# Kernel optimization log

Measured on AMD Instinct MI355X. Metric: run time of the kernel, lower is better.

Reference implementation:

```python
import jax, jax.numpy as jnp
import numpy as np

B, K, T, C = 4, 8, 2048, 64

def setup_inputs() -> dict:
    key = jax.random.key(0)
    ks = jax.random.split(key, 7)
    return {
        "x": jax.random.normal(ks[0], (B, K, T, C), dtype=jnp.float32),
        "Wq": jax.random.normal(ks[1], (C, C), dtype=jnp.float32) / np.sqrt(C),
        "bq": jax.random.normal(ks[2], (C,), dtype=jnp.float32) * 0.01,
        "Wk": jax.random.normal(ks[3], (C, C), dtype=jnp.float32) / np.sqrt(C),
        "bk": jax.random.normal(ks[4], (C,), dtype=jnp.float32) * 0.01,
        "Wv": jax.random.normal(ks[5], (C, C), dtype=jnp.float32) / np.sqrt(C),
        "bv": jax.random.normal(ks[6], (C,), dtype=jnp.float32) * 0.01,
    }

def reference(x, Wq, bq, Wk, bk, Wv, bv):
    c_dim = x.shape[-1]
    # torch nn.Linear: y = x @ W.T + b
    q = jnp.einsum('bktc,dc->bktd', x, Wq) + bq
    k = jnp.einsum('bktc,dc->bktd', x, Wk) + bk
    v = jnp.einsum('bktc,dc->bktd', x, Wv) + bv
    scores = jnp.einsum('bkic,bkjc->bkij', q, k) / jnp.sqrt(jnp.float32(c_dim))
    attn = jax.nn.softmax(scores, axis=-1)
    out = jnp.einsum('bkij,bkjc->bkic', attn, v)
    return out
```

## Files before the change

kernel.cpp:

```cpp
#include <hip/hip_runtime.h>


#define T_DIM 2048
#define NHEAD 32
#define HSTRIDE (T_DIM * 64)
#define QSCALE 0.18033688011112042f
#define SOFF  8.0f

#define SWZ(row, grp) ((row) * 64 + ((((grp) ^ ((row) & 7)) & 7) * 8))

typedef _Float16 h8 __attribute__((ext_vector_type(8)));
typedef _Float16 h4 __attribute__((ext_vector_type(4)));
typedef __fp16   g2 __attribute__((ext_vector_type(2)));
typedef float    f4 __attribute__((ext_vector_type(4)));

union H4U { h4 v; g2 p[2]; };
union H8U { h8 v; h4 h[2]; };

#if defined(__has_builtin)
#if __has_builtin(__builtin_amdgcn_exp2f)
#define EXP2(x) __builtin_amdgcn_exp2f(x)
#endif
#endif
#ifndef EXP2
__device__ inline float exp2_raw(float x) {
    float r;
    asm("v_exp_f32 %0, %1" : "=v"(r) : "v"(x));
    return r;
}
#define EXP2(x) exp2_raw(x)
#endif

__device__ inline h4 cvt4(f4 x) {
    H4U u;
    u.p[0] = __builtin_amdgcn_cvt_pkrtz(x[0], x[1]);
    u.p[1] = __builtin_amdgcn_cvt_pkrtz(x[2], x[3]);
    return u.v;
}

__global__ __launch_bounds__(256) void qkv_proj_kernel(
    const float* __restrict__ x,
    const float* __restrict__ Wq, const float* __restrict__ bq,
    const float* __restrict__ Wk, const float* __restrict__ bk,
    const float* __restrict__ Wv, const float* __restrict__ bv,
    _Float16* __restrict__ qh, _Float16* __restrict__ khT,
    _Float16* __restrict__ vtT)
{
    __shared__ _Float16 ws[3][64 * 64];
    __shared__ _Float16 xs[64 * 64];
    __shared__ float bsh[3][64];
    _Float16* ot = xs;

    const int tid  = threadIdx.x;
    const int row0 = blockIdx.x * 64;
    const int head = blockIdx.x >> 5;
    const int t0   = (blockIdx.x & 31) * 64;

    #pragma unroll
    for (int m = 0; m < 3; ++m) {
        const float* Wm = (m == 0) ? Wq : ((m == 1) ? Wk : Wv);
        const float* bm = (m == 0) ? bq : ((m == 1) ? bk : bv);
        #pragma unroll
        for (int pass = 0; pass < 4; ++pass) {
            const int idx = pass * 1024 + tid * 4;
            const int d = idx >> 6, c = idx & 63;
            f4 wv = *(const f4*)(Wm + idx);
            *(h4*)&ws[m][SWZ(d, c >> 3) + (c & 7)] = cvt4(wv);
        }
        if (tid < 64) bsh[m][tid] = bm[tid];
    }
    {
        const float* xb = x + (size_t)row0 * 64;
        #pragma unroll
        for (int pass = 0; pass < 4; ++pass) {
            const int idx = pass * 1024 + tid * 4;
            const int r = idx >> 6, c = idx & 63;
            f4 xv = *(const f4*)(xb + idx);
            *(h4*)&xs[SWZ(r, c >> 3) + (c & 7)] = cvt4(xv);
        }
    }
    __syncthreads();

    const int w    = tid >> 6;
    const int lane = tid & 63;
    const int l15  = lane & 15;
    const int qd   = lane >> 4;

    h8 af[2];
    #pragma unroll
    for (int ch = 0; ch < 2; ++ch)
        af[ch] = *(const h8*)&xs[SWZ(w * 16 + l15, ch * 4 + qd)];

    #pragma unroll
    for (int m = 0; m < 3; ++m) {
        h8 bf[4][2];
        #pragma unroll
        for (int ns = 0; ns < 4; ++ns)
            #pragma unroll
            for (int ch = 0; ch < 2; ++ch)
                bf[ns][ch] = *(const h8*)&ws[m][SWZ(ns * 16 + l15, ch * 4 + qd)];

        f4 acc[4];
        #pragma unroll
        for (int ns = 0; ns < 4; ++ns)
            acc[ns] = (f4){0.f, 0.f, 0.f, 0.f};
        #pragma unroll
        for (int ch = 0; ch < 2; ++ch)
            #pragma unroll
            for (int ns = 0; ns < 4; ++ns)
                acc[ns] = __builtin_amdgcn_mfma_f32_16x16x32_f16(
                    af[ch], bf[ns][ch], acc[ns], 0, 0, 0);

        __syncthreads();
        if (m < 2) {
            #pragma unroll
            for (int ns = 0; ns < 4; ++ns) {
                const int d = ns * 16 + l15;
                const float bias = bsh[m][d];
                #pragma unroll
                for (int r = 0; r < 4; ++r) {
                    const int t = w * 16 + qd * 4 + r;
                    float v = acc[ns][r] + bias;
                    if (m == 0) v *= QSCALE;
                    ot[SWZ(t, d >> 3) + (d & 7)] = (_Float16)v;
                }
            }
            __syncthreads();
            if (m == 0) {
                #pragma unroll
                for (int pass = 0; pass < 2; ++pass) {
                    const int t  = pass * 32 + (tid >> 3);
                    const int c0 = (tid & 7) * 8;
                    *(h8*)&qh[(size_t)(row0 + t) * 64 + c0] =
                        *(const h8*)&ot[SWZ(t, tid & 7)];
                }
            } else {
                #pragma unroll
                for (int pass = 0; pass < 2; ++pass) {
                    const int f    = pass * 2048 + tid * 8;
                    const int Jl   = f >> 10;
                    const int rest = f & 1023;
                    const int ch_  = rest >> 9;
                    const int qd_  = (rest >> 7) & 3;
                    const int l15_ = (rest >> 3) & 15;
                    h8 val = *(const h8*)&ot[SWZ(Jl * 16 + l15_, ch_ * 4 + qd_)];
                    *(h8*)&khT[(size_t)head * HSTRIDE + ((t0 >> 4) + Jl) * 1024 + rest] = val;
                }
            }
        } else {
            #pragma unroll
            for (int ns = 0; ns < 4; ++ns) {
                const int d = ns * 16 + l15;
                const float bias = bsh[2][d];
                const int tl = w * 16 + qd * 4;
                f4 pvf;
                #pragma unroll
                for (int r = 0; r < 4; ++r)
                    pvf[r] = acc[ns][r] + bias;
                *(h4*)&ot[SWZ(d, tl >> 3) + (tl & 7)] = cvt4(pvf);
            }
            __syncthreads();
            #pragma unroll
            for (int pass = 0; pass < 2; ++pass) {
                const int f   = pass * 2048 + tid * 8;
                const int qd3 = f >> 10;
                const int rem = f & 1023;
                const int c   = rem >> 4;
                const int g   = (rem & 15) >> 3;
                const int ta  = (2 * g) * 16 + qd3 * 4;
                const int tb  = ta + 16;
                H8U val;
                val.h[0] = *(const h4*)&ot[SWZ(c, ta >> 3) + (ta & 7)];
                val.h[1] = *(const h4*)&ot[SWZ(c, tb >> 3) + (tb & 7)];
                *(h8*)&vtT[(size_t)head * HSTRIDE + (t0 >> 6) * 4096 + f] = val.v;
            }
        }
    }
}

__global__ __launch_bounds__(256, 2) void attn_kernel(
    const _Float16* __restrict__ qh, const _Float16* __restrict__ khT,
    const _Float16* __restrict__ vtT, float* __restrict__ out)
{
    __shared__ float mrg[2][64][41];
    const int tid  = threadIdx.x;
    const int w    = tid >> 6;
    const int lane = tid & 63;
    const int l15  = lane & 15;
    const int qd   = lane >> 4;
    const int qgrp = w >> 1;
    const int kph  = w & 1;

    const int bid  = blockIdx.x;
    const int xcd  = bid & 7;
    const int slot = bid >> 3;
    const int head = xcd * 4 + (slot >> 5);
    const int q0   = (slot & 31) * 64 + qgrp * 32;

    h8 qf[2][2];
    #pragma unroll
    for (int is = 0; is < 2; ++is) {
        const _Float16* qp = qh + (size_t)(head * T_DIM + q0 + is * 16 + l15) * 64 + qd * 8;
        qf[is][0] = *(const h8*)qp;
        qf[is][1] = *(const h8*)(qp + 32);
    }

    const h4 vones = {(_Float16)1.0f, (_Float16)1.0f, (_Float16)1.0f, (_Float16)1.0f};
    f4 lacc[2] = {(f4){0.f,0.f,0.f,0.f}, (f4){0.f,0.f,0.f,0.f}};
    f4 oacc[2][4];
    #pragma unroll
    for (int is = 0; is < 2; ++is)
        #pragma unroll
        for (int cs = 0; cs < 4; ++cs)
            oacc[is][cs] = (f4){0.f, 0.f, 0.f, 0.f};

    const _Float16* kA = khT + (size_t)head * HSTRIDE + kph * 65536;
    const _Float16* kB = kA + 2048;
    const _Float16* vA = vtT + (size_t)head * HSTRIDE + kph * 65536;
    const int ko = lane * 8;
    const int vo = qd * 1024 + l15 * 16;

    h8 kf[4][2];
    #pragma unroll
    for (int jt = 0; jt < 4; ++jt)
        #pragma unroll
        for (int ch = 0; ch < 2; ++ch)
            kf[jt][ch] = *(const h8*)(((jt < 2) ? kA : kB) + (jt & 1) * 1024 + ch * 512 + ko);

    for (int kt = 0; kt < 16; ++kt) {
        H8U vf8[4][2];
        #pragma unroll
        for (int cs = 0; cs < 4; ++cs) {
            vf8[cs][0].v = *(const h8*)(vA + cs * 256 + vo);
            vf8[cs][1].v = *(const h8*)(vA + cs * 256 + vo + 8);
        }

        f4 st[4][2];
        #pragma unroll
        for (int jt = 0; jt < 4; ++jt)
            #pragma unroll
            for (int is = 0; is < 2; ++is)
                st[jt][is] = (f4){-SOFF, -SOFF, -SOFF, -SOFF};
        #pragma unroll
        for (int ch = 0; ch < 2; ++ch)
            #pragma unroll
            for (int jt = 0; jt < 4; ++jt)
                #pragma unroll
                for (int is = 0; is < 2; ++is)
                    st[jt][is] = __builtin_amdgcn_mfma_f32_16x16x32_f16(
                        kf[jt][ch], qf[is][ch], st[jt][is], 0, 0, 0);

        kA += 4096; kB += 4096;
        if (kt < 15) {
            #pragma unroll
            for (int jt = 0; jt < 4; ++jt)
                #pragma unroll
                for (int ch = 0; ch < 2; ++ch)
                    kf[jt][ch] = *(const h8*)(((jt < 2) ? kA : kB) + (jt & 1) * 1024 + ch * 512 + ko);
        }

        h4 pf[4][2];
        #pragma unroll
        for (int is = 0; is < 2; ++is)
            #pragma unroll
            for (int jt = 0; jt < 4; ++jt) {
                f4 p;
                p[0] = EXP2(st[jt][is][0]);
                p[1] = EXP2(st[jt][is][1]);
                p[2] = EXP2(st[jt][is][2]);
                p[3] = EXP2(st[jt][is][3]);
                pf[jt][is] = cvt4(p);
            }

        #pragma unroll
        for (int jt = 0; jt < 4; ++jt) {
            #pragma unroll
            for (int cs = 0; cs < 4; ++cs)
                #pragma unroll
                for (int is = 0; is < 2; ++is)
                    oacc[is][cs] = __builtin_amdgcn_mfma_f32_16x16x16f16(
                        pf[jt][is], vf8[cs][jt >> 1].h[jt & 1], oacc[is][cs], 0, 0, 0);
            #pragma unroll
            for (int is = 0; is < 2; ++is)
                lacc[is] = __builtin_amdgcn_mfma_f32_16x16x16f16(
                    pf[jt][is], vones, lacc[is], 0, 0, 0);
        }
        vA += 4096;
    }

    if (kph == 1) {
        #pragma unroll
        for (int is = 0; is < 2; ++is) {
            #pragma unroll
            for (int cs = 0; cs < 4; ++cs)
                #pragma unroll
                for (int r = 0; r < 4; ++r)
                    mrg[qgrp][lane][(is * 4 + cs) * 4 + r] = oacc[is][cs][r];
            #pragma unroll
            for (int r = 0; r < 4; ++r)
                mrg[qgrp][lane][32 + is * 4 + r] = lacc[is][r];
        }
    }
    __syncthreads();
    if (kph == 0) {
        #pragma unroll
        for (int is = 0; is < 2; ++is) {
            float linv[4];
            #pragma unroll
            for (int r = 0; r < 4; ++r)
                linv[r] = 1.f / (lacc[is][r] + mrg[qgrp][lane][32 + is * 4 + r]);
            #pragma unroll
            for (int cs = 0; cs < 4; ++cs) {
                const int c = cs * 16 + l15;
                #pragma unroll
                for (int r = 0; r < 4; ++r) {
                    const int t = q0 + is * 16 + qd * 4 + r;
                    float o = oacc[is][cs][r] + mrg[qgrp][lane][(is * 4 + cs) * 4 + r];
                    out[(size_t)(head * T_DIM + t) * 64 + c] = o * linv[r];
                }
            }
        }
    }
}

extern "C" void kernel_launch(void* const* d_in, const int* in_sizes, int n_in,
                              void* d_out, int out_size, void* d_ws, size_t ws_size,
                              hipStream_t stream)
{
    (void)in_sizes; (void)n_in; (void)out_size; (void)ws_size;
    const float* x  = (const float*)d_in[0];
    const float* Wq = (const float*)d_in[1];
    const float* bq = (const float*)d_in[2];
    const float* Wk = (const float*)d_in[3];
    const float* bk = (const float*)d_in[4];
    const float* Wv = (const float*)d_in[5];
    const float* bv = (const float*)d_in[6];
    float* out = (float*)d_out;

    _Float16* qh  = (_Float16*)d_ws;
    _Float16* khT = qh + (size_t)NHEAD * HSTRIDE;
    _Float16* vtT = khT + (size_t)NHEAD * HSTRIDE;

    hipLaunchKernelGGL(qkv_proj_kernel, dim3(1024), dim3(256), 0, stream,
                       x, Wq, bq, Wk, bk, Wv, bv, qh, khT, vtT);
    hipLaunchKernelGGL(attn_kernel, dim3(1024), dim3(256), 0, stream,
                       qh, khT, vtT, out);
}
```

Before: 131.0 us.

## Split attention key range across four waves per query group and load x directly

The attention kernel now launches 512 threads per block, so each query group has four waves, each handling a quarter of the key sequence (8 tiles instead of 16). Partial outputs and row sums are merged through shared memory in three sequential rounds. The aim is shorter per-wave serial loops and more waves in flight to hide latency, at the cost of more merge synchronisation and register pressure under the 512-thread launch bound. Separately, the QKV projection loads x straight from global memory into MFMA fragments instead of staging it through shared memory.

```diff
diff --git a/kernel.cpp b/kernel.cpp
--- a/kernel.cpp
+++ b/kernel.cpp
@@ -38,6 +38,13 @@
     return u.v;
 }
 
+__device__ inline h8 cvt8(f4 a, f4 b) {
+    H8U r;
+    r.h[0] = cvt4(a);
+    r.h[1] = cvt4(b);
+    return r.v;
+}
+
 __global__ __launch_bounds__(256) void qkv_proj_kernel(
     const float* __restrict__ x,
     const float* __restrict__ Wq, const float* __restrict__ bq,
@@ -47,9 +54,8 @@
     _Float16* __restrict__ vtT)
 {
     __shared__ _Float16 ws[3][64 * 64];
-    __shared__ _Float16 xs[64 * 64];
+    __shared__ _Float16 ot[64 * 64];
     __shared__ float bsh[3][64];
-    _Float16* ot = xs;
 
     const int tid  = threadIdx.x;
     const int row0 = blockIdx.x * 64;
@@ -69,17 +75,6 @@
         }
         if (tid < 64) bsh[m][tid] = bm[tid];
     }
-    {
-        const float* xb = x + (size_t)row0 * 64;
-        #pragma unroll
-        for (int pass = 0; pass < 4; ++pass) {
-            const int idx = pass * 1024 + tid * 4;
-            const int r = idx >> 6, c = idx & 63;
-            f4 xv = *(const f4*)(xb + idx);
-            *(h4*)&xs[SWZ(r, c >> 3) + (c & 7)] = cvt4(xv);
-        }
-    }
-    __syncthreads();
 
     const int w    = tid >> 6;
     const int lane = tid & 63;
@@ -87,9 +82,16 @@
     const int qd   = lane >> 4;
 
     h8 af[2];
-    #pragma unroll
-    for (int ch = 0; ch < 2; ++ch)
-        af[ch] = *(const h8*)&xs[SWZ(w * 16 + l15, ch * 4 + qd)];
+    {
+        const float* xp = x + (size_t)(row0 + w * 16 + l15) * 64 + qd * 8;
+        #pragma unroll
+        for (int ch = 0; ch < 2; ++ch) {
+            f4 a0 = *(const f4*)(xp + ch * 32);
+            f4 a1 = *(const f4*)(xp + ch * 32 + 4);
+            af[ch] = cvt8(a0, a1);
+        }
+    }
+    __syncthreads();
 
     #pragma unroll
     for (int m = 0; m < 3; ++m) {
@@ -178,7 +180,7 @@
     }
 }
 
-__global__ __launch_bounds__(256, 2) void attn_kernel(
+__global__ __launch_bounds__(512, 2) void attn_kernel(
     const _Float16* __restrict__ qh, const _Float16* __restrict__ khT,
     const _Float16* __restrict__ vtT, float* __restrict__ out)
 {
@@ -188,8 +190,8 @@
     const int lane = tid & 63;
     const int l15  = lane & 15;
     const int qd   = lane >> 4;
-    const int qgrp = w >> 1;
-    const int kph  = w & 1;
+    const int qgrp = w & 1;
+    const int kph  = w >> 1;
 
     const int bid  = blockIdx.x;
     const int xcd  = bid & 7;
@@ -214,9 +216,9 @@
         for (int cs = 0; cs < 4; ++cs)
             oacc[is][cs] = (f4){0.f, 0.f, 0.f, 0.f};
 
-    const _Float16* kA = khT + (size_t)head * HSTRIDE + kph * 65536;
+    const _Float16* kA = khT + (size_t)head * HSTRIDE + kph * 32768;
     const _Float16* kB = kA + 2048;
-    const _Float16* vA = vtT + (size_t)head * HSTRIDE + kph * 65536;
+    const _Float16* vA = vtT + (size_t)head * HSTRIDE + kph * 32768;
     const int ko = lane * 8;
     const int vo = qd * 1024 + l15 * 16;
 
@@ -227,7 +229,7 @@
         for (int ch = 0; ch < 2; ++ch)
             kf[jt][ch] = *(const h8*)(((jt < 2) ? kA : kB) + (jt & 1) * 1024 + ch * 512 + ko);
 
-    for (int kt = 0; kt < 16; ++kt) {
+    for (int kt = 0; kt < 8; ++kt) {
         H8U vf8[4][2];
         #pragma unroll
         for (int cs = 0; cs < 4; ++cs) {
@@ -251,7 +253,7 @@
                         kf[jt][ch], qf[is][ch], st[jt][is], 0, 0, 0);
 
         kA += 4096; kB += 4096;
-        if (kt < 15) {
+        if (kt < 7) {
             #pragma unroll
             for (int jt = 0; jt < 4; ++jt)
                 #pragma unroll
@@ -288,35 +290,52 @@
         vA += 4096;
     }
 
-    if (kph == 1) {
-        #pragma unroll
-        for (int is = 0; is < 2; ++is) {
-            #pragma unroll
-            for (int cs = 0; cs < 4; ++cs)
+    #pragma unroll
+    for (int src = 3; src >= 1; --src) {
+        if (kph == src) {
+            #pragma unroll
+            for (int is = 0; is < 2; ++is) {
+                #pragma unroll
+                for (int cs = 0; cs < 4; ++cs)
+                    #pragma unroll
+                    for (int r = 0; r < 4; ++r)
+                        mrg[qgrp][lane][(is * 4 + cs) * 4 + r] = oacc[is][cs][r];
                 #pragma unroll
                 for (int r = 0; r < 4; ++r)
-                    mrg[qgrp][lane][(is * 4 + cs) * 4 + r] = oacc[is][cs][r];
-            #pragma unroll
-            for (int r = 0; r < 4; ++r)
-                mrg[qgrp][lane][32 + is * 4 + r] = lacc[is][r];
-        }
-    }
-    __syncthreads();
+                    mrg[qgrp][lane][32 + is * 4 + r] = lacc[is][r];
+            }
+        }
+        __syncthreads();
+        if (kph == 0) {
+            #pragma unroll
+            for (int is = 0; is < 2; ++is) {
+                #pragma unroll
+                for (int cs = 0; cs < 4; ++cs)
+                    #pragma unroll
+                    for (int r = 0; r < 4; ++r)
+                        oacc[is][cs][r] += mrg[qgrp][lane][(is * 4 + cs) * 4 + r];
+                #pragma unroll
+                for (int r = 0; r < 4; ++r)
+                    lacc[is][r] += mrg[qgrp][lane][32 + is * 4 + r];
+            }
+        }
+        if (src > 1) __syncthreads();
+    }
+
     if (kph == 0) {
         #pragma unroll
         for (int is = 0; is < 2; ++is) {
             float linv[4];
             #pragma unroll
             for (int r = 0; r < 4; ++r)
-                linv[r] = 1.f / (lacc[is][r] + mrg[qgrp][lane][32 + is * 4 + r]);
+                linv[r] = 1.f / lacc[is][r];
             #pragma unroll
             for (int cs = 0; cs < 4; ++cs) {
                 const int c = cs * 16 + l15;
                 #pragma unroll
                 for (int r = 0; r < 4; ++r) {
                     const int t = q0 + is * 16 + qd * 4 + r;
-                    float o = oacc[is][cs][r] + mrg[qgrp][lane][(is * 4 + cs) * 4 + r];
-                    out[(size_t)(head * T_DIM + t) * 64 + c] = o * linv[r];
+                    out[(size_t)(head * T_DIM + t) * 64 + c] = oacc[is][cs][r] * linv[r];
                 }
             }
         }
@@ -343,6 +362,6 @@
 
     hipLaunchKernelGGL(qkv_proj_kernel, dim3(1024), dim3(256), 0, stream,
                        x, Wq, bq, Wk, bk, Wv, bv, qh, khT, vtT);
-    hipLaunchKernelGGL(attn_kernel, dim3(1024), dim3(256), 0, stream,
+    hipLaunchKernelGGL(attn_kernel, dim3(1024), dim3(512), 0, stream,
                        qh, khT, vtT, out);
 }
```

New measurement: 132.9 us. About the same (+1.5%).

## Switch attention to 32x32x16 MFMA tiles with shuffled P fragments and new K/V layouts

Applied to the files above, without the earlier changes.

Rewrites the attention inner loop to use 32x32x16 f16 MFMA for both QK^T and PV. The P fragment is rebuilt via lane-xor-32 shuffles instead of going through LDS, and the row sum is computed with scalar adds instead of an extra ones-MFMA. The projection kernel writes K and V in new tile layouts matching the 32x32 operand order and loads x straight from global into registers. Occupancy hint rises to 3 blocks per CU. The larger tiles cut instruction count and drop the ones-MFMA, but the shuffles and selects add VALU work and register pressure.

```diff
diff --git a/kernel.cpp b/kernel.cpp
--- a/kernel.cpp
+++ b/kernel.cpp
@@ -13,9 +13,12 @@
 typedef _Float16 h4 __attribute__((ext_vector_type(4)));
 typedef __fp16   g2 __attribute__((ext_vector_type(2)));
 typedef float    f4 __attribute__((ext_vector_type(4)));
+typedef float    f16v __attribute__((ext_vector_type(16)));
 
 union H4U { h4 v; g2 p[2]; };
 union H8U { h8 v; h4 h[2]; };
+union PKU { g2 g; unsigned u; };
+union FRU { h8 v; unsigned u[4]; };
 
 #if defined(__has_builtin)
 #if __has_builtin(__builtin_amdgcn_exp2f)
@@ -38,6 +41,13 @@
     return u.v;
 }
 
+__device__ inline h8 cvt8(f4 a, f4 b) {
+    H8U r;
+    r.h[0] = cvt4(a);
+    r.h[1] = cvt4(b);
+    return r.v;
+}
+
 __global__ __launch_bounds__(256) void qkv_proj_kernel(
     const float* __restrict__ x,
     const float* __restrict__ Wq, const float* __restrict__ bq,
@@ -47,14 +57,13 @@
     _Float16* __restrict__ vtT)
 {
     __shared__ _Float16 ws[3][64 * 64];
-    __shared__ _Float16 xs[64 * 64];
+    __shared__ _Float16 ot[64 * 64];
     __shared__ float bsh[3][64];
-    _Float16* ot = xs;
 
     const int tid  = threadIdx.x;
     const int row0 = blockIdx.x * 64;
     const int head = blockIdx.x >> 5;
-    const int t0   = (blockIdx.x & 31) * 64;
+    const int kt0  = blockIdx.x & 31;
 
     #pragma unroll
     for (int m = 0; m < 3; ++m) {
@@ -69,17 +78,6 @@
         }
         if (tid < 64) bsh[m][tid] = bm[tid];
     }
-    {
-        const float* xb = x + (size_t)row0 * 64;
-        #pragma unroll
-        for (int pass = 0; pass < 4; ++pass) {
-            const int idx = pass * 1024 + tid * 4;
-            const int r = idx >> 6, c = idx & 63;
-            f4 xv = *(const f4*)(xb + idx);
-            *(h4*)&xs[SWZ(r, c >> 3) + (c & 7)] = cvt4(xv);
-        }
-    }
-    __syncthreads();
 
     const int w    = tid >> 6;
     const int lane = tid & 63;
@@ -87,9 +85,16 @@
     const int qd   = lane >> 4;
 
     h8 af[2];
-    #pragma unroll
-    for (int ch = 0; ch < 2; ++ch)
-        af[ch] = *(const h8*)&xs[SWZ(w * 16 + l15, ch * 4 + qd)];
+    {
+        const float* xp = x + (size_t)(row0 + w * 16 + l15) * 64 + qd * 8;
+        #pragma unroll
+        for (int ch = 0; ch < 2; ++ch) {
+            f4 a0 = *(const f4*)(xp + ch * 32);
+            f4 a1 = *(const f4*)(xp + ch * 32 + 4);
+            af[ch] = cvt8(a0, a1);
+        }
+    }
+    __syncthreads();
 
     #pragma unroll
     for (int m = 0; m < 3; ++m) {
@@ -137,14 +142,14 @@
             } else {
                 #pragma unroll
                 for (int pass = 0; pass < 2; ++pass) {
-                    const int f    = pass * 2048 + tid * 8;
-                    const int Jl   = f >> 10;
-                    const int rest = f & 1023;
-                    const int ch_  = rest >> 9;
-                    const int qd_  = (rest >> 7) & 3;
-                    const int l15_ = (rest >> 3) & 15;
-                    h8 val = *(const h8*)&ot[SWZ(Jl * 16 + l15_, ch_ * 4 + qd_)];
-                    *(h8*)&khT[(size_t)head * HSTRIDE + ((t0 >> 4) + Jl) * 1024 + rest] = val;
+                    const int f  = pass * 2048 + tid * 8;
+                    const int r  = f >> 9;
+                    const int l  = (f >> 3) & 63;
+                    const int jb = r >> 2, kc = r & 3;
+                    const int jl = jb * 32 + (l & 31);
+                    const int cg = kc * 2 + (l >> 5);
+                    h8 val = *(const h8*)&ot[SWZ(jl, cg)];
+                    *(h8*)&khT[(size_t)head * HSTRIDE + kt0 * 4096 + f] = val;
                 }
             }
         } else {
@@ -162,32 +167,29 @@
             __syncthreads();
             #pragma unroll
             for (int pass = 0; pass < 2; ++pass) {
-                const int f   = pass * 2048 + tid * 8;
-                const int qd3 = f >> 10;
-                const int rem = f & 1023;
-                const int c   = rem >> 4;
-                const int g   = (rem & 15) >> 3;
-                const int ta  = (2 * g) * 16 + qd3 * 4;
-                const int tb  = ta + 16;
-                H8U val;
-                val.h[0] = *(const h4*)&ot[SWZ(c, ta >> 3) + (ta & 7)];
-                val.h[1] = *(const h4*)&ot[SWZ(c, tb >> 3) + (tb & 7)];
-                *(h8*)&vtT[(size_t)head * HSTRIDE + (t0 >> 6) * 4096 + f] = val.v;
-            }
-        }
-    }
-}
-
-__global__ __launch_bounds__(256, 2) void attn_kernel(
+                const int f  = pass * 2048 + tid * 8;
+                const int r  = f >> 9;
+                const int l  = (f >> 3) & 63;
+                const int jc = r >> 1, cb = r & 1;
+                const int c  = cb * 32 + (l & 31);
+                const int tg = jc * 2 + (l >> 5);
+                h8 val = *(const h8*)&ot[SWZ(c, tg)];
+                *(h8*)&vtT[(size_t)head * HSTRIDE + kt0 * 4096 + f] = val;
+            }
+        }
+    }
+}
+
+__global__ __launch_bounds__(256, 3) void attn_kernel(
     const _Float16* __restrict__ qh, const _Float16* __restrict__ khT,
     const _Float16* __restrict__ vtT, float* __restrict__ out)
 {
-    __shared__ float mrg[2][64][41];
+    __shared__ float mrg[2][64][33];
     const int tid  = threadIdx.x;
     const int w    = tid >> 6;
     const int lane = tid & 63;
-    const int l15  = lane & 15;
-    const int qd   = lane >> 4;
+    const int i32  = lane & 31;
+    const int hl   = lane >> 5;
     const int qgrp = w >> 1;
     const int kph  = w & 1;
 
@@ -197,128 +199,123 @@
     const int head = xcd * 4 + (slot >> 5);
     const int q0   = (slot & 31) * 64 + qgrp * 32;
 
-    h8 qf[2][2];
+    h8 qf[4];
+    {
+        const _Float16* qp = qh + (size_t)(head * T_DIM + q0 + i32) * 64 + hl * 8;
+        #pragma unroll
+        for (int kc = 0; kc < 4; ++kc)
+            qf[kc] = *(const h8*)(qp + kc * 16);
+    }
+
+    f16v oacc[2];
     #pragma unroll
-    for (int is = 0; is < 2; ++is) {
-        const _Float16* qp = qh + (size_t)(head * T_DIM + q0 + is * 16 + l15) * 64 + qd * 8;
-        qf[is][0] = *(const h8*)qp;
-        qf[is][1] = *(const h8*)(qp + 32);
-    }
-
-    const h4 vones = {(_Float16)1.0f, (_Float16)1.0f, (_Float16)1.0f, (_Float16)1.0f};
-    f4 lacc[2] = {(f4){0.f,0.f,0.f,0.f}, (f4){0.f,0.f,0.f,0.f}};
-    f4 oacc[2][4];
+    for (int cb = 0; cb < 2; ++cb)
+        #pragma unroll
+        for (int e = 0; e < 16; ++e)
+            oacc[cb][e] = 0.f;
+    float lsum = 0.f;
+
+    const _Float16* kA = khT + (size_t)head * HSTRIDE + kph * 16 * 4096;
+    const _Float16* kB = kA + 2048;
+    const _Float16* vA = vtT + (size_t)head * HSTRIDE + kph * 16 * 4096;
+    const _Float16* vB = vA + 2048;
+    const int ko = lane * 8;
+
+    h8 kf[8];
     #pragma unroll
-    for (int is = 0; is < 2; ++is)
-        #pragma unroll
-        for (int cs = 0; cs < 4; ++cs)
-            oacc[is][cs] = (f4){0.f, 0.f, 0.f, 0.f};
-
-    const _Float16* kA = khT + (size_t)head * HSTRIDE + kph * 65536;
-    const _Float16* kB = kA + 2048;
-    const _Float16* vA = vtT + (size_t)head * HSTRIDE + kph * 65536;
-    const int ko = lane * 8;
-    const int vo = qd * 1024 + l15 * 16;
-
-    h8 kf[4][2];
-    #pragma unroll
-    for (int jt = 0; jt < 4; ++jt)
-        #pragma unroll
-        for (int ch = 0; ch < 2; ++ch)
-            kf[jt][ch] = *(const h8*)(((jt < 2) ? kA : kB) + (jt & 1) * 1024 + ch * 512 + ko);
+    for (int r = 0; r < 8; ++r)
+        kf[r] = *(const h8*)(((r < 4) ? kA : kB) + (r & 3) * 512 + ko);
 
     for (int kt = 0; kt < 16; ++kt) {
-        H8U vf8[4][2];
-        #pragma unroll
-        for (int cs = 0; cs < 4; ++cs) {
-            vf8[cs][0].v = *(const h8*)(vA + cs * 256 + vo);
-            vf8[cs][1].v = *(const h8*)(vA + cs * 256 + vo + 8);
-        }
-
-        f4 st[4][2];
-        #pragma unroll
-        for (int jt = 0; jt < 4; ++jt)
-            #pragma unroll
-            for (int is = 0; is < 2; ++is)
-                st[jt][is] = (f4){-SOFF, -SOFF, -SOFF, -SOFF};
-        #pragma unroll
-        for (int ch = 0; ch < 2; ++ch)
-            #pragma unroll
-            for (int jt = 0; jt < 4; ++jt)
-                #pragma unroll
-                for (int is = 0; is < 2; ++is)
-                    st[jt][is] = __builtin_amdgcn_mfma_f32_16x16x32_f16(
-                        kf[jt][ch], qf[is][ch], st[jt][is], 0, 0, 0);
+        h8 vf[8];
+        #pragma unroll
+        for (int r = 0; r < 8; ++r)
+            vf[r] = *(const h8*)(((r < 4) ? vA : vB) + (r & 3) * 512 + ko);
+
+        f16v st[2];
+        #pragma unroll
+        for (int jb = 0; jb < 2; ++jb)
+            #pragma unroll
+            for (int e = 0; e < 16; ++e)
+                st[jb][e] = -SOFF;
+        #pragma unroll
+        for (int kc = 0; kc < 4; ++kc)
+            #pragma unroll
+            for (int jb = 0; jb < 2; ++jb)
+                st[jb] = __builtin_amdgcn_mfma_f32_32x32x16_f16(
+                    kf[jb * 4 + kc], qf[kc], st[jb], 0, 0, 0);
 
         kA += 4096; kB += 4096;
         if (kt < 15) {
             #pragma unroll
-            for (int jt = 0; jt < 4; ++jt)
-                #pragma unroll
-                for (int ch = 0; ch < 2; ++ch)
-                    kf[jt][ch] = *(const h8*)(((jt < 2) ? kA : kB) + (jt & 1) * 1024 + ch * 512 + ko);
-        }
-
-        h4 pf[4][2];
-        #pragma unroll
-        for (int is = 0; is < 2; ++is)
-            #pragma unroll
-            for (int jt = 0; jt < 4; ++jt) {
-                f4 p;
-                p[0] = EXP2(st[jt][is][0]);
-                p[1] = EXP2(st[jt][is][1]);
-                p[2] = EXP2(st[jt][is][2]);
-                p[3] = EXP2(st[jt][is][3]);
-                pf[jt][is] = cvt4(p);
-            }
-
-        #pragma unroll
-        for (int jt = 0; jt < 4; ++jt) {
-            #pragma unroll
-            for (int cs = 0; cs < 4; ++cs)
-                #pragma unroll
-                for (int is = 0; is < 2; ++is)
-                    oacc[is][cs] = __builtin_amdgcn_mfma_f32_16x16x16f16(
-                        pf[jt][is], vf8[cs][jt >> 1].h[jt & 1], oacc[is][cs], 0, 0, 0);
-            #pragma unroll
-            for (int is = 0; is < 2; ++is)
-                lacc[is] = __builtin_amdgcn_mfma_f32_16x16x16f16(
-                    pf[jt][is], vones, lacc[is], 0, 0, 0);
-        }
-        vA += 4096;
-    }
+            for (int r = 0; r < 8; ++r)
+                kf[r] = *(const h8*)(((r < 4) ? kA : kB) + (r & 3) * 512 + ko);
+        }
+
+        #pragma unroll
+        for (int jb = 0; jb < 2; ++jb) {
+            float p[16];
+            #pragma unroll
+            for (int e = 0; e < 16; ++e)
+                p[e] = EXP2(st[jb][e]);
+            float s0 = 0.f, s1 = 0.f;
+            #pragma unroll
+            for (int e = 0; e < 8; ++e) { s0 += p[e]; s1 += p[8 + e]; }
+            lsum += s0 + s1;
+
+            #pragma unroll
+            for (int jh = 0; jh < 2; ++jh) {
+                PKU a0, a1, b0, b1;
+                a0.g = __builtin_amdgcn_cvt_pkrtz(p[8 * jh + 0], p[8 * jh + 1]);
+                a1.g = __builtin_amdgcn_cvt_pkrtz(p[8 * jh + 2], p[8 * jh + 3]);
+                b0.g = __builtin_amdgcn_cvt_pkrtz(p[8 * jh + 4], p[8 * jh + 5]);
+                b1.g = __builtin_amdgcn_cvt_pkrtz(p[8 * jh + 6], p[8 * jh + 7]);
+                unsigned xa0 = (unsigned)__shfl_xor((int)a0.u, 32, 64);
+                unsigned xa1 = (unsigned)__shfl_xor((int)a1.u, 32, 64);
+                unsigned xb0 = (unsigned)__shfl_xor((int)b0.u, 32, 64);
+                unsigned xb1 = (unsigned)__shfl_xor((int)b1.u, 32, 64);
+                FRU frag;
+                frag.u[0] = hl ? xb0 : a0.u;
+                frag.u[1] = hl ? xb1 : a1.u;
+                frag.u[2] = hl ? b0.u : xa0;
+                frag.u[3] = hl ? b1.u : xa1;
+                const int jc = jb * 2 + jh;
+                oacc[0] = __builtin_amdgcn_mfma_f32_32x32x16_f16(
+                    frag.v, vf[jc * 2 + 0], oacc[0], 0, 0, 0);
+                oacc[1] = __builtin_amdgcn_mfma_f32_32x32x16_f16(
+                    frag.v, vf[jc * 2 + 1], oacc[1], 0, 0, 0);
+            }
+        }
+        vA += 4096; vB += 4096;
+    }
+
+    float lx = lsum + __shfl_xor(lsum, 32, 64);
 
     if (kph == 1) {
-        #pragma unroll
-        for (int is = 0; is < 2; ++is) {
-            #pragma unroll
-            for (int cs = 0; cs < 4; ++cs)
-                #pragma unroll
-                for (int r = 0; r < 4; ++r)
-                    mrg[qgrp][lane][(is * 4 + cs) * 4 + r] = oacc[is][cs][r];
-            #pragma unroll
-            for (int r = 0; r < 4; ++r)
-                mrg[qgrp][lane][32 + is * 4 + r] = lacc[is][r];
-        }
+        float* pm = &mrg[qgrp][lane][0];
+        #pragma unroll
+        for (int cb = 0; cb < 2; ++cb)
+            #pragma unroll
+            for (int e = 0; e < 16; ++e)
+                pm[cb * 16 + e] = oacc[cb][e];
+        pm[32] = lx;
     }
     __syncthreads();
     if (kph == 0) {
-        #pragma unroll
-        for (int is = 0; is < 2; ++is) {
-            float linv[4];
-            #pragma unroll
-            for (int r = 0; r < 4; ++r)
-                linv[r] = 1.f / (lacc[is][r] + mrg[qgrp][lane][32 + is * 4 + r]);
-            #pragma unroll
-            for (int cs = 0; cs < 4; ++cs) {
-                const int c = cs * 16 + l15;
-                #pragma unroll
-                for (int r = 0; r < 4; ++r) {
-                    const int t = q0 + is * 16 + qd * 4 + r;
-                    float o = oacc[is][cs][r] + mrg[qgrp][lane][(is * 4 + cs) * 4 + r];
-                    out[(size_t)(head * T_DIM + t) * 64 + c] = o * linv[r];
-                }
-            }
+        const float* pm = &mrg[qgrp][lane][0];
+        #pragma unroll
+        for (int cb = 0; cb < 2; ++cb)
+            #pragma unroll
+            for (int e = 0; e < 16; ++e)
+                oacc[cb][e] += pm[cb * 16 + e];
+        const float linv_i = 1.f / (lx + pm[32]);
+        #pragma unroll
+        for (int e = 0; e < 16; ++e) {
+            const int ir = (e & 3) + 8 * (e >> 2) + 4 * hl;
+            const float li = __shfl(linv_i, ir, 64);
+            const size_t rowoff = (size_t)(head * T_DIM + q0 + ir) * 64 + i32;
+            out[rowoff]      = oacc[0][e] * li;
+            out[rowoff + 32] = oacc[1][e] * li;
         }
     }
 }
```

New measurement: 139.6 us. 6.6% more time.

## Software-pipeline QK^T scores one tile ahead and load x fragments directly

Applied to the files above, without the earlier changes.

The attention loop is restructured so that the score MFMAs for the next key tile are issued before the PV MFMAs of the current tile, and V fragments are prefetched one iteration ahead. This is meant to overlap the exp2 and convert work and the global load latency with matrix work. In the projection kernel, x is loaded straight from global memory into register fragments instead of being staged through swizzled LDS. The cost is more live registers (stN, prefetched vf8), which may lower occupancy, and uncoalesced direct loads of x.

```diff
diff --git a/kernel.cpp b/kernel.cpp
--- a/kernel.cpp
+++ b/kernel.cpp
@@ -38,6 +38,13 @@
     return u.v;
 }
 
+__device__ inline h8 cvt8(f4 a, f4 b) {
+    H8U r;
+    r.h[0] = cvt4(a);
+    r.h[1] = cvt4(b);
+    return r.v;
+}
+
 __global__ __launch_bounds__(256) void qkv_proj_kernel(
     const float* __restrict__ x,
     const float* __restrict__ Wq, const float* __restrict__ bq,
@@ -47,9 +54,8 @@
     _Float16* __restrict__ vtT)
 {
     __shared__ _Float16 ws[3][64 * 64];
-    __shared__ _Float16 xs[64 * 64];
+    __shared__ _Float16 ot[64 * 64];
     __shared__ float bsh[3][64];
-    _Float16* ot = xs;
 
     const int tid  = threadIdx.x;
     const int row0 = blockIdx.x * 64;
@@ -69,17 +75,6 @@
         }
         if (tid < 64) bsh[m][tid] = bm[tid];
     }
-    {
-        const float* xb = x + (size_t)row0 * 64;
-        #pragma unroll
-        for (int pass = 0; pass < 4; ++pass) {
-            const int idx = pass * 1024 + tid * 4;
-            const int r = idx >> 6, c = idx & 63;
-            f4 xv = *(const f4*)(xb + idx);
-            *(h4*)&xs[SWZ(r, c >> 3) + (c & 7)] = cvt4(xv);
-        }
-    }
-    __syncthreads();
 
     const int w    = tid >> 6;
     const int lane = tid & 63;
@@ -87,9 +82,16 @@
     const int qd   = lane >> 4;
 
     h8 af[2];
-    #pragma unroll
-    for (int ch = 0; ch < 2; ++ch)
-        af[ch] = *(const h8*)&xs[SWZ(w * 16 + l15, ch * 4 + qd)];
+    {
+        const float* xp = x + (size_t)(row0 + w * 16 + l15) * 64 + qd * 8;
+        #pragma unroll
+        for (int ch = 0; ch < 2; ++ch) {
+            f4 a0 = *(const f4*)(xp + ch * 32);
+            f4 a1 = *(const f4*)(xp + ch * 32 + 4);
+            af[ch] = cvt8(a0, a1);
+        }
+    }
+    __syncthreads();
 
     #pragma unroll
     for (int m = 0; m < 3; ++m) {
@@ -226,39 +228,36 @@
         #pragma unroll
         for (int ch = 0; ch < 2; ++ch)
             kf[jt][ch] = *(const h8*)(((jt < 2) ? kA : kB) + (jt & 1) * 1024 + ch * 512 + ko);
+    H8U vf8[4][2];
+    #pragma unroll
+    for (int cs = 0; cs < 4; ++cs) {
+        vf8[cs][0].v = *(const h8*)(vA + cs * 256 + vo);
+        vf8[cs][1].v = *(const h8*)(vA + cs * 256 + vo + 8);
+    }
+
+    f4 st[4][2];
+    #pragma unroll
+    for (int jt = 0; jt < 4; ++jt)
+        #pragma unroll
+        for (int is = 0; is < 2; ++is)
+            st[jt][is] = (f4){-SOFF, -SOFF, -SOFF, -SOFF};
+    #pragma unroll
+    for (int ch = 0; ch < 2; ++ch)
+        #pragma unroll
+        for (int jt = 0; jt < 4; ++jt)
+            #pragma unroll
+            for (int is = 0; is < 2; ++is)
+                st[jt][is] = __builtin_amdgcn_mfma_f32_16x16x32_f16(
+                    kf[jt][ch], qf[is][ch], st[jt][is], 0, 0, 0);
+
+    kA += 4096; kB += 4096;
+    #pragma unroll
+    for (int jt = 0; jt < 4; ++jt)
+        #pragma unroll
+        for (int ch = 0; ch < 2; ++ch)
+            kf[jt][ch] = *(const h8*)(((jt < 2) ? kA : kB) + (jt & 1) * 1024 + ch * 512 + ko);
 
     for (int kt = 0; kt < 16; ++kt) {
-        H8U vf8[4][2];
-        #pragma unroll
-        for (int cs = 0; cs < 4; ++cs) {
-            vf8[cs][0].v = *(const h8*)(vA + cs * 256 + vo);
-            vf8[cs][1].v = *(const h8*)(vA + cs * 256 + vo + 8);
-        }
-
-        f4 st[4][2];
-        #pragma unroll
-        for (int jt = 0; jt < 4; ++jt)
-            #pragma unroll
-            for (int is = 0; is < 2; ++is)
-                st[jt][is] = (f4){-SOFF, -SOFF, -SOFF, -SOFF};
-        #pragma unroll
-        for (int ch = 0; ch < 2; ++ch)
-            #pragma unroll
-            for (int jt = 0; jt < 4; ++jt)
-                #pragma unroll
-                for (int is = 0; is < 2; ++is)
-                    st[jt][is] = __builtin_amdgcn_mfma_f32_16x16x32_f16(
-                        kf[jt][ch], qf[is][ch], st[jt][is], 0, 0, 0);
-
-        kA += 4096; kB += 4096;
-        if (kt < 15) {
-            #pragma unroll
-            for (int jt = 0; jt < 4; ++jt)
-                #pragma unroll
-                for (int ch = 0; ch < 2; ++ch)
-                    kf[jt][ch] = *(const h8*)(((jt < 2) ? kA : kB) + (jt & 1) * 1024 + ch * 512 + ko);
-        }
-
         h4 pf[4][2];
         #pragma unroll
         for (int is = 0; is < 2; ++is)
@@ -272,20 +271,64 @@
                 pf[jt][is] = cvt4(p);
             }
 
-        #pragma unroll
-        for (int jt = 0; jt < 4; ++jt) {
-            #pragma unroll
-            for (int cs = 0; cs < 4; ++cs)
+        f4 stN[4][2];
+        if (kt < 15) {
+            #pragma unroll
+            for (int jt = 0; jt < 4; ++jt)
                 #pragma unroll
                 for (int is = 0; is < 2; ++is)
-                    oacc[is][cs] = __builtin_amdgcn_mfma_f32_16x16x16f16(
-                        pf[jt][is], vf8[cs][jt >> 1].h[jt & 1], oacc[is][cs], 0, 0, 0);
+                    stN[jt][is] = (f4){-SOFF, -SOFF, -SOFF, -SOFF};
+            #pragma unroll
+            for (int ch = 0; ch < 2; ++ch)
+                #pragma unroll
+                for (int jt = 0; jt < 4; ++jt)
+                    #pragma unroll
+                    for (int is = 0; is < 2; ++is)
+                        stN[jt][is] = __builtin_amdgcn_mfma_f32_16x16x32_f16(
+                            kf[jt][ch], qf[is][ch], stN[jt][is], 0, 0, 0);
+            kA += 4096; kB += 4096;
+            if (kt < 14) {
+                #pragma unroll
+                for (int jt = 0; jt < 4; ++jt)
+                    #pragma unroll
+                    for (int ch = 0; ch < 2; ++ch)
+                        kf[jt][ch] = *(const h8*)(((jt < 2) ? kA : kB) + (jt & 1) * 1024 + ch * 512 + ko);
+            }
+        }
+
+        #pragma unroll
+        for (int cs = 0; cs < 4; ++cs)
+            #pragma unroll
+            for (int is = 0; is < 2; ++is) {
+                oacc[is][cs] = __builtin_amdgcn_mfma_f32_16x16x16f16(
+                    pf[0][is], vf8[cs][0].h[0], oacc[is][cs], 0, 0, 0);
+                oacc[is][cs] = __builtin_amdgcn_mfma_f32_16x16x16f16(
+                    pf[1][is], vf8[cs][0].h[1], oacc[is][cs], 0, 0, 0);
+                oacc[is][cs] = __builtin_amdgcn_mfma_f32_16x16x16f16(
+                    pf[2][is], vf8[cs][1].h[0], oacc[is][cs], 0, 0, 0);
+                oacc[is][cs] = __builtin_amdgcn_mfma_f32_16x16x16f16(
+                    pf[3][is], vf8[cs][1].h[1], oacc[is][cs], 0, 0, 0);
+            }
+        #pragma unroll
+        for (int jt = 0; jt < 4; ++jt)
             #pragma unroll
             for (int is = 0; is < 2; ++is)
                 lacc[is] = __builtin_amdgcn_mfma_f32_16x16x16f16(
                     pf[jt][is], vones, lacc[is], 0, 0, 0);
-        }
+
         vA += 4096;
+        if (kt < 15) {
+            #pragma unroll
+            for (int cs = 0; cs < 4; ++cs) {
+                vf8[cs][0].v = *(const h8*)(vA + cs * 256 + vo);
+                vf8[cs][1].v = *(const h8*)(vA + cs * 256 + vo + 8);
+            }
+            #pragma unroll
+            for (int jt = 0; jt < 4; ++jt)
+                #pragma unroll
+                for (int is = 0; is < 2; ++is)
+                    st[jt][is] = stN[jt][is];
+        }
     }
 
     if (kph == 1) {
```

Result: no change. 131.2 us (+0.2%).
